# Optimization experiments

Measured on AMD Instinct MI355X. Metric: run time of the kernel, lower is better.

The kernel has to match this reference:

```python
import jax, jax.numpy as jnp
import numpy as np

N = 100000   # nodes
E = 1200000  # edges
D = 64       # input_dim
H = 64       # hidden_dim
L = 4        # num_layers (GIN layers)
G = 128      # graphs in batch
BN_EPS = 1e-5


def setup_inputs() -> dict:
    key = jax.random.key(0)
    ks = jax.random.split(key, 8)
    x = jax.random.normal(ks[0], (N, D), dtype=jnp.float32)
    edge_index = jax.random.randint(ks[1], (2, E), 0, N)
    batch = jnp.sort(jax.random.randint(ks[2], (N,), 0, G))
    s = 1.0 / np.sqrt(H).astype(np.float32)
    W_emb = jax.random.normal(ks[3], (D, H), dtype=jnp.float32) * s
    b_emb = jnp.zeros((H,), jnp.float32)
    W1 = jax.random.normal(ks[4], (L, H, H), dtype=jnp.float32) * s
    b1 = jnp.zeros((L, H), jnp.float32)
    gamma = jnp.ones((L, H), jnp.float32)
    beta = jnp.zeros((L, H), jnp.float32)
    W2 = jax.random.normal(ks[5], (L, H, H), dtype=jnp.float32) * s
    b2 = jnp.zeros((L, H), jnp.float32)
    return dict(x=x, edge_index=edge_index, batch=batch, W_emb=W_emb, b_emb=b_emb,
                W1=W1, b1=b1, gamma=gamma, beta=beta, W2=W2, b2=b2)


def _mean_pool(h, batch):
    # global_mean_pool: segment sum / segment count, fixed num_segments=G
    s = jax.ops.segment_sum(h, batch, num_segments=G)
    cnt = jax.ops.segment_sum(jnp.ones((h.shape[0],), h.dtype), batch, num_segments=G)
    return s / jnp.maximum(cnt, 1.0)[:, None]


def _bn(h, g, b):
    # BatchNorm1d in training mode: batch statistics, biased variance
    mu = h.mean(axis=0)
    var = h.var(axis=0)
    return g * (h - mu) * jax.lax.rsqrt(var + BN_EPS) + b


def reference(x, edge_index, batch, W_emb, b_emb, W1, b1, gamma, beta, W2, b2):
    src, dst = edge_index[0], edge_index[1]
    h = x @ W_emb + b_emb                      # [N, H] embedding_h
    reps = [_mean_pool(h, batch)]
    for i in range(L):
        # GINConv, eps=0: mlp((1+eps)*x + sum_{j in N(i)} x_j)
        agg = jax.ops.segment_sum(h[src], dst, num_segments=N)
        z = h + agg
        # 2-layer MLP: Linear -> BN -> ReLU -> Linear
        z = jax.nn.relu(_bn(z @ W1[i] + b1[i], gamma[i], beta[i]))
        h = z @ W2[i] + b2[i]
        reps.append(_mean_pool(h, batch))
    return jnp.concatenate(reps, axis=1)       # [G, H*(L+1)]
```

## Files before the change

### kernel.cpp

```cpp
#include <hip/hip_runtime.h>
#include <hip/hip_bf16.h>

typedef __hip_bfloat16 bf16;
typedef unsigned short u16;
typedef unsigned int u32;
typedef __attribute__((ext_vector_type(8))) short short8;
typedef __attribute__((ext_vector_type(8))) unsigned short ushort8;
typedef __attribute__((ext_vector_type(4))) float f32x4;

#define N_NODES 100000
#define N_EDGES 1200000
#define DIM 64
#define NG 128
#define NLAYERS 4
#define BN_EPS 1e-5f

#define BKT_BITS 9
#define BKT 512
#define NBKT ((N_NODES + BKT - 1) / BKT)
#define SCAT_BLK 128
#define SCAT_CH ((N_EDGES + SCAT_BLK - 1) / SCAT_BLK)
#define CSR_CAP 8192

#define WS_GSUM   0
#define WS_GSUMSQ 64
#define WS_AB     128
#define WS_FLAG   256
#define WS_GB     320
#define WS_WALL   512
#define OFF_WEMB  0
#define OFF_BEMB  4096
#define OFF_W1    4160
#define OFF_B1    20544
#define OFF_GAMMA 20800
#define OFF_BETA  21056
#define OFF_W2    21312
#define OFF_B2    37696
#define W_TOTAL   37952
#define WS_PACC8  38464
#define WS_WPK    104000
#define WS_CUR    204000
#define WS_ROWPTR 304128
#define WS_CSR    404160
#define WS_Z      1604160
#define WS_H      4804160
#define WS_PAIR   8004160
#define WS_END    9204160
#define WS_NEED_BYTES ((size_t)WS_END * 4)

#define NBLK   ((N_NODES + 63) / 64)

__device__ __forceinline__ float us2f(unsigned short u) {
    return __uint_as_float(((u32)u) << 16);
}
__device__ __forceinline__ short f2bs(float f) {
    bf16 b = __float2bfloat16(f);
    u16 u; __builtin_memcpy(&u, &b, 2);
    return (short)u;
}

__device__ __forceinline__ float loadf(const void* p, long i, int flag) {
    if (flag) return ((const float*)p)[i];
    u32 w = ((u32)((const u16*)p)[i]) << 16;
    return __uint_as_float(w);
}

__global__ void k_diag(u32* out, float val) {
    if (threadIdx.x == 0 && blockIdx.x == 0) {
        bf16 b = __float2bfloat16(val);
        u16 bits;
        __builtin_memcpy(&bits, &b, 2);
        u32 w = ((u32)bits << 16) | bits;
        for (int i = 0; i < 8; i++) out[i] = w;
    }
}

__global__ void k_detect(const void* x, int* flag) {
    if (threadIdx.x == 0 && blockIdx.x == 0) {
        const u16* u = (const u16*)x;
        int bad = 0;
        for (int i = 0; i < 512; i++) {
            float v = __uint_as_float(((u32)u[i]) << 16);
            if (!(fabsf(v) < 100.f)) bad++;
        }
        *flag = (bad > 16) ? 1 : 0;
    }
}

__global__ __launch_bounds__(256) void k_convert(const void* W_emb, const void* b_emb,
                                                 const void* W1, const void* b1,
                                                 const void* gamma, const void* beta,
                                                 const void* W2, const void* b2,
                                                 const int* flagp, float* dst) {
    int f = *flagp;
    for (int i = blockIdx.x * blockDim.x + threadIdx.x; i < W_TOTAL;
         i += gridDim.x * blockDim.x) {
        const void* p; int off;
        if (i < OFF_BEMB)       { p = W_emb; off = i; }
        else if (i < OFF_W1)    { p = b_emb; off = i - OFF_BEMB; }
        else if (i < OFF_B1)    { p = W1;    off = i - OFF_W1; }
        else if (i < OFF_GAMMA) { p = b1;    off = i - OFF_B1; }
        else if (i < OFF_BETA)  { p = gamma; off = i - OFF_GAMMA; }
        else if (i < OFF_W2)    { p = beta;  off = i - OFF_BETA; }
        else if (i < OFF_B2)    { p = W2;    off = i - OFF_W2; }
        else                    { p = b2;    off = i - OFF_B2; }
        dst[i] = loadf(p, off, f);
    }
}

__global__ __launch_bounds__(256) void k_pack(const float* __restrict__ wall,
                                              u16* __restrict__ wpk) {
    int i = blockIdx.x * 256 + threadIdx.x;
    if (i >= 9 * 4096) return;
    int m = i >> 12, r = i & 4095;
    int j = r & 7, l = (r >> 3) & 63, cc = (r >> 9) & 3, kk = r >> 11;
    int d = kk * 32 + ((l >> 4) << 3) + j;
    int c = cc * 16 + (l & 15);
    int moff = (m == 0) ? OFF_WEMB
             : (m <= 4 ? OFF_W1 + (m - 1) * 4096 : OFF_W2 + (m - 5) * 4096);
    wpk[i] = (u16)f2bs(wall[moff + d * 64 + c]);
}

__global__ void k_gbounds(const int* __restrict__ batch, int* __restrict__ gb) {
    int t = threadIdx.x;
    if (t <= NG) {
        int a = 0, b = N_NODES;
        while (a < b) { int m = (a + b) >> 1; if (batch[m] < t) a = m + 1; else b = m; }
        gb[t] = a;
    }
}


__global__ __launch_bounds__(256) void k_bhist(const int* __restrict__ ei,
                                               int* __restrict__ bhist) {
    __shared__ int hl[NBKT];
    int tid = threadIdx.x;
    for (int b = tid; b < NBKT; b += 256) hl[b] = 0;
    __syncthreads();
    for (int e = blockIdx.x * 256 + tid; e < N_EDGES; e += gridDim.x * 256)
        atomicAdd(&hl[ei[N_EDGES + e] >> BKT_BITS], 1);
    __syncthreads();
    for (int b = tid; b < NBKT; b += 256)
        if (hl[b]) atomicAdd(&bhist[b], hl[b]);
}

__global__ __launch_bounds__(256) void k_bscan(const int* __restrict__ bhist,
                                               int* __restrict__ boff,
                                               int* __restrict__ bcur) {
    __shared__ int s[256];
    int tid = threadIdx.x;
    int v = (tid < NBKT) ? bhist[tid] : 0;
    s[tid] = v;
    __syncthreads();
    for (int off = 1; off < 256; off <<= 1) {
        int t = (tid >= off) ? s[tid - off] : 0;
        __syncthreads();
        s[tid] += t;
        __syncthreads();
    }
    if (tid < NBKT) { int e = s[tid] - v; boff[tid] = e; bcur[tid] = e; }
    if (tid == 0) boff[NBKT] = s[255];
}

__global__ __launch_bounds__(256) void k_bscatter(const int* __restrict__ ei,
                                                  int* __restrict__ bcur,
                                                  u32* __restrict__ pair) {
    __shared__ int cnt[NBKT];
    int tid = threadIdx.x;
    int cbeg = blockIdx.x * SCAT_CH;
    int cend = cbeg + SCAT_CH; if (cend > N_EDGES) cend = N_EDGES;
    for (int b = tid; b < NBKT; b += 256) cnt[b] = 0;
    __syncthreads();
    for (int e = cbeg + tid; e < cend; e += 256)
        atomicAdd(&cnt[ei[N_EDGES + e] >> BKT_BITS], 1);
    __syncthreads();
    for (int b = tid; b < NBKT; b += 256) {
        int c = cnt[b];
        cnt[b] = c ? atomicAdd(&bcur[b], c) : 0;
    }
    __syncthreads();
    for (int e = cbeg + tid; e < cend; e += 256) {
        int s = ei[e];
        int d = ei[N_EDGES + e];
        int pos = atomicAdd(&cnt[d >> BKT_BITS], 1);
        pair[pos] = (u32)s | ((u32)(d & (BKT - 1)) << 17);
    }
}

__global__ __launch_bounds__(256) void k_bcsr(const u32* __restrict__ pair,
                                              const int* __restrict__ boff,
                                              int* __restrict__ rowptr,
                                              int* __restrict__ csr) {
    __shared__ int degl[BKT];
    __shared__ int offl[BKT];
    __shared__ int sc[256];
    __shared__ int csrl[CSR_CAP];
    int b = blockIdx.x, tid = threadIdx.x;
    int nbase = b << BKT_BITS;
    int nodes = N_NODES - nbase; if (nodes > BKT) nodes = BKT;
    int p0 = boff[b], p1 = boff[b + 1];
    int span = p1 - p0;
    for (int i = tid; i < BKT; i += 256) degl[i] = 0;
    __syncthreads();
    for (int p = p0 + tid; p < p1; p += 256)
        atomicAdd(&degl[pair[p] >> 17], 1);
    __syncthreads();
    int a0 = degl[2 * tid], a1 = degl[2 * tid + 1];
    sc[tid] = a0 + a1;
    __syncthreads();
    for (int off = 1; off < 256; off <<= 1) {
        int t = (tid >= off) ? sc[tid - off] : 0;
        __syncthreads();
        sc[tid] += t;
        __syncthreads();
    }
    int base = sc[tid] - (a0 + a1);
    offl[2 * tid] = base;
    offl[2 * tid + 1] = base + a0;
    __syncthreads();
    for (int i = tid; i < nodes; i += 256) rowptr[nbase + i] = p0 + offl[i];
    if (b == NBKT - 1 && tid == 0) rowptr[N_NODES] = p1;
    for (int i = tid; i < BKT; i += 256) degl[i] = offl[i];
    __syncthreads();
    if (span <= CSR_CAP) {
        for (int p = p0 + tid; p < p1; p += 256) {
            u32 pk = pair[p];
            int pos = atomicAdd(&degl[pk >> 17], 1);
            csrl[pos] = (int)(pk & 0x1FFFFu);
        }
        __syncthreads();
        for (int i = tid; i < span; i += 256) csr[p0 + i] = csrl[i];
    } else {
        for (int p = p0 + tid; p < p1; p += 256) {
            u32 pk = pair[p];
            int pos = atomicAdd(&degl[pk >> 17], 1);
            csr[p0 + pos] = (int)(pk & 0x1FFFFu);
        }
    }
}


__global__ __launch_bounds__(256) void k_deghist(const int* __restrict__ rowptr,
                                                 int* __restrict__ dhist) {
    __shared__ int hl[256];
    int tid = threadIdx.x;
    hl[tid] = 0;
    __syncthreads();
    for (int i = blockIdx.x * 256 + tid; i < N_NODES; i += gridDim.x * 256) {
        int d = rowptr[i + 1] - rowptr[i];
        int b = 255 - (d > 255 ? 255 : d);
        atomicAdd(&hl[b], 1);
    }
    __syncthreads();
    if (hl[tid]) atomicAdd(&dhist[tid], hl[tid]);
}

__global__ void k_degscan(const int* __restrict__ dhist, int* __restrict__ dhcur,
                          int* __restrict__ perm) {
    __shared__ int s[256];
    int tid = threadIdx.x;
    int v = dhist[tid];
    s[tid] = v;
    __syncthreads();
    for (int off = 1; off < 256; off <<= 1) {
        int t = (tid >= off) ? s[tid - off] : 0;
        __syncthreads();
        s[tid] += t;
        __syncthreads();
    }
    dhcur[tid] = s[tid] - v;
    if (tid < NBLK * 64 - N_NODES) perm[N_NODES + tid] = N_NODES;
}

__global__ __launch_bounds__(256) void k_degfill(const int* __restrict__ rowptr,
                                                 int* __restrict__ dhcur,
                                                 int* __restrict__ perm) {
    __shared__ int cnt[256];
    int tid = threadIdx.x;
    int chunk = (N_NODES + gridDim.x - 1) / gridDim.x;
    int beg = blockIdx.x * chunk;
    int end = beg + chunk; if (end > N_NODES) end = N_NODES;
    cnt[tid] = 0;
    __syncthreads();
    for (int i = beg + tid; i < end; i += 256) {
        int d = rowptr[i + 1] - rowptr[i];
        int b = 255 - (d > 255 ? 255 : d);
        atomicAdd(&cnt[b], 1);
    }
    __syncthreads();
    int c = cnt[tid];
    cnt[tid] = c ? atomicAdd(&dhcur[tid], c) : 0;
    __syncthreads();
    for (int i = beg + tid; i < end; i += 256) {
        int d = rowptr[i + 1] - rowptr[i];
        int b = 255 - (d > 255 ? 255 : d);
        int pos = atomicAdd(&cnt[b], 1);
        perm[pos] = i;
    }
}

__device__ __forceinline__ void store_tile(u16* cb, const f32x4* acc, bf16* out,
                                           int base, int wv, int lane) {
    int r15 = lane & 15, half = lane >> 4;
#pragma unroll
    for (int cc = 0; cc < 4; cc++) {
#pragma unroll
        for (int r = 0; r < 4; r++) {
            int trow = half * 4 + r;
            int idx = (trow * 64 + cc * 16 + r15) ^ ((trow & 7) << 3);
            cb[idx] = (u16)f2bs(acc[cc][r]);
        }
    }
#pragma unroll
    for (int p = 0; p < 2; p++) {
        int trow = lane >> 2;
        int o = (trow * 64 + (lane & 3) * 8 + p * 32) ^ ((trow & 7) << 3);
        short8 val = *(const short8*)&cb[o];
        int grow = base + (wv << 4) + trow;
        if (grow < N_NODES)
            *(short8*)((u16*)out + (long)grow * 64 + (lane & 3) * 8 + p * 32) = val;
    }
}

__device__ __forceinline__ void store_tile_p(u16* cb, const f32x4* acc, bf16* out,
                                             const int* pl, int wv, int lane) {
    int r15 = lane & 15, half = lane >> 4;
#pragma unroll
    for (int cc = 0; cc < 4; cc++) {
#pragma unroll
        for (int r = 0; r < 4; r++) {
            int trow = half * 4 + r;
            int idx = (trow * 64 + cc * 16 + r15) ^ ((trow & 7) << 3);
            cb[idx] = (u16)f2bs(acc[cc][r]);
        }
    }
#pragma unroll
    for (int p = 0; p < 2; p++) {
        int trow = lane >> 2;
        int o = (trow * 64 + (lane & 3) * 8 + p * 32) ^ ((trow & 7) << 3);
        short8 val = *(const short8*)&cb[o];
        int grow = pl[(wv << 4) + trow];
        if (grow < N_NODES)
            *(short8*)((u16*)out + (long)grow * 64 + (lane & 3) * 8 + p * 32) = val;
    }
}

__global__ __launch_bounds__(256) void k_embed(const void* __restrict__ x,
                                               const int* __restrict__ flagp,
                                               const u16* __restrict__ wpk,
                                               const float* __restrict__ bf_,
                                               bf16* __restrict__ h) {
    __shared__ u16 cbuf[4 * 1024];
    int tid = threadIdx.x, lane = tid & 63, wv = tid >> 6;
    int r15 = lane & 15, half = lane >> 4;
    int f = *flagp;
    int base = blockIdx.x * 64;
    int row = base + (wv << 4) + r15;
    bool valid = row < N_NODES;

    float xv[16];
#pragma unroll
    for (int j = 0; j < 16; j++) xv[j] = 0.f;
    if (valid) {
        if (f) {
            const f32x4* xp = (const f32x4*)((const float*)x + (long)row * 64 + half * 8);
            f32x4 u0 = xp[0], u1 = xp[1], w0 = xp[8], w1 = xp[9];
#pragma unroll
            for (int j = 0; j < 4; j++) {
                xv[j] = u0[j]; xv[4 + j] = u1[j];
                xv[8 + j] = w0[j]; xv[12 + j] = w1[j];
            }
        } else {
            const ushort8* xp = (const ushort8*)((const u16*)x + (long)row * 64 + half * 8);
            ushort8 s0 = xp[0], s1 = xp[4];
#pragma unroll
            for (int j = 0; j < 8; j++) { xv[j] = us2f(s0[j]); xv[8 + j] = us2f(s1[j]); }
        }
    }
    short8 A0, A1;
#pragma unroll
    for (int j = 0; j < 8; j++) { A0[j] = f2bs(xv[j]); A1[j] = f2bs(xv[8 + j]); }

    const short8* Wp = (const short8*)wpk;
    short8 Bw[8];
#pragma unroll
    for (int i = 0; i < 8; i++) Bw[i] = Wp[i * 64 + lane];
    f32x4 acc[4];
#pragma unroll
    for (int cc = 0; cc < 4; cc++) {
        float bb = bf_[cc * 16 + r15];
        acc[cc] = (f32x4){bb, bb, bb, bb};
        acc[cc] = __builtin_amdgcn_mfma_f32_16x16x32_bf16(A0, Bw[cc], acc[cc], 0, 0, 0);
        acc[cc] = __builtin_amdgcn_mfma_f32_16x16x32_bf16(A1, Bw[4 + cc], acc[cc], 0, 0, 0);
    }
    store_tile(cbuf + wv * 1024, acc, h, base, wv, lane);
}

__global__ __launch_bounds__(256) void k_layer1(const bf16* __restrict__ h,
                                                const int* __restrict__ rowptr,
                                                const int* __restrict__ csr,
                                                const int* __restrict__ perm,
                                                bf16* __restrict__ z,
                                                const u16* __restrict__ wpk,
                                                const float* __restrict__ bf_,
                                                float* __restrict__ gsum,
                                                float* __restrict__ gsumsq) {
    __shared__ u16 cbuf[4 * 1024];
    __shared__ float psum[DIM], psq[DIM];
    __shared__ int pl[64];
    int tid = threadIdx.x, lane = tid & 63, wv = tid >> 6;
    int r15 = lane & 15, half = lane >> 4;
    int base = blockIdx.x * 64;

    if (tid < DIM) { psum[tid] = 0.f; psq[tid] = 0.f; }
    if (tid < 64) pl[tid] = perm[base + tid];
    __syncthreads();

    int row = pl[(wv << 4) + r15];
    bool valid = row < N_NODES;

    float v[16];
#pragma unroll
    for (int j = 0; j < 16; j++) v[j] = 0.f;
    int p0 = 0, dg = 0;
    if (valid) {
        p0 = rowptr[row];
        dg = rowptr[row + 1] - p0;
        const ushort8* hp = (const ushort8*)((const u16*)h + (long)row * 64 + half * 8);
        ushort8 s0 = hp[0], s1 = hp[4];
#pragma unroll
        for (int j = 0; j < 8; j++) { v[j] = us2f(s0[j]); v[8 + j] = us2f(s1[j]); }
    }
    const int* cp = csr + p0;
    int t = 0;
    int n0 = 0, n1 = 0, n2 = 0, n3 = 0;
    if (4 <= dg) { n0 = cp[0]; n1 = cp[1]; n2 = cp[2]; n3 = cp[3]; }
    while (t + 4 <= dg) {
        const ushort8* q0 = (const ushort8*)((const u16*)h + (long)n0 * 64 + half * 8);
        const ushort8* q1 = (const ushort8*)((const u16*)h + (long)n1 * 64 + half * 8);
        const ushort8* q2 = (const ushort8*)((const u16*)h + (long)n2 * 64 + half * 8);
        const ushort8* q3 = (const ushort8*)((const u16*)h + (long)n3 * 64 + half * 8);
        ushort8 a0 = q0[0], b0 = q0[4];
        ushort8 a1 = q1[0], b1 = q1[4];
        ushort8 a2 = q2[0], b2 = q2[4];
        ushort8 a3 = q3[0], b3 = q3[4];
        t += 4;
        if (t + 4 <= dg) { n0 = cp[t]; n1 = cp[t + 1]; n2 = cp[t + 2]; n3 = cp[t + 3]; }
#pragma unroll
        for (int j = 0; j < 8; j++) {
            v[j]     += (us2f(a0[j]) + us2f(a1[j])) + (us2f(a2[j]) + us2f(a3[j]));
            v[8 + j] += (us2f(b0[j]) + us2f(b1[j])) + (us2f(b2[j]) + us2f(b3[j]));
        }
    }
    for (; t < dg; t++) {
        int s = cp[t];
        const ushort8* q = (const ushort8*)((const u16*)h + (long)s * 64 + half * 8);
        ushort8 a = q[0], b = q[4];
#pragma unroll
        for (int j = 0; j < 8; j++) { v[j] += us2f(a[j]); v[8 + j] += us2f(b[j]); }
    }

    short8 A0, A1;
#pragma unroll
    for (int j = 0; j < 8; j++) { A0[j] = f2bs(v[j]); A1[j] = f2bs(v[8 + j]); }

    const short8* Wp = (const short8*)wpk;
    short8 Bw[8];
#pragma unroll
    for (int i = 0; i < 8; i++) Bw[i] = Wp[i * 64 + lane];
    f32x4 acc[4];
#pragma unroll
    for (int cc = 0; cc < 4; cc++) {
        float bb = bf_[cc * 16 + r15];
        acc[cc] = (f32x4){bb, bb, bb, bb};
        acc[cc] = __builtin_amdgcn_mfma_f32_16x16x32_bf16(A0, Bw[cc], acc[cc], 0, 0, 0);
        acc[cc] = __builtin_amdgcn_mfma_f32_16x16x32_bf16(A1, Bw[4 + cc], acc[cc], 0, 0, 0);
    }

#pragma unroll
    for (int cc = 0; cc < 4; cc++) {
        float s = 0.f, q = 0.f;
#pragma unroll
        for (int r = 0; r < 4; r++) {
            int prow = pl[(wv << 4) + half * 4 + r];
            if (prow < N_NODES) { float val = acc[cc][r]; s += val; q += val * val; }
        }
        s += __shfl_xor(s, 16, 64); s += __shfl_xor(s, 32, 64);
        q += __shfl_xor(q, 16, 64); q += __shfl_xor(q, 32, 64);
        if (half == 0) {
            atomicAdd(&psum[cc * 16 + r15], s);
            atomicAdd(&psq[cc * 16 + r15], q);
        }
    }

    store_tile_p(cbuf + wv * 1024, acc, z, pl, wv, lane);

    __syncthreads();
    if (tid < DIM) {
        atomicAdd(&gsum[tid], psum[tid]);
        atomicAdd(&gsumsq[tid], psq[tid]);
    }
}

__global__ void k_stats(const float* __restrict__ gsum, const float* __restrict__ gsumsq,
                        const float* __restrict__ gamma_f, const float* __restrict__ beta_f,
                        float* __restrict__ ab) {
    int c = threadIdx.x;
    if (c < DIM) {
        float inv_n = 1.0f / (float)N_NODES;
        float mu = gsum[c] * inv_n;
        float var = fmaxf(gsumsq[c] * inv_n - mu * mu, 0.f);
        float a = gamma_f[c] * rsqrtf(var + BN_EPS);
        ab[c] = a;
        ab[DIM + c] = beta_f[c] - mu * a;
    }
}

__global__ __launch_bounds__(256) void k_gemm2(const bf16* __restrict__ z,
                                               bf16* __restrict__ h,
                                               const u16* __restrict__ wpk,
                                               const float* __restrict__ bf_,
                                               const float* __restrict__ ab) {
    __shared__ u16 cbuf[4 * 1024];
    int tid = threadIdx.x, lane = tid & 63, wv = tid >> 6;
    int r15 = lane & 15, half = lane >> 4;
    int base = blockIdx.x * 64;
    int row = base + (wv << 4) + r15;
    bool valid = row < N_NODES;

    const f32x4* ap = (const f32x4*)ab;
    f32x4 A0v = ap[half * 2], A1v = ap[half * 2 + 1];
    f32x4 A2v = ap[8 + half * 2], A3v = ap[8 + half * 2 + 1];
    f32x4 S0v = ap[16 + half * 2], S1v = ap[16 + half * 2 + 1];
    f32x4 S2v = ap[24 + half * 2], S3v = ap[24 + half * 2 + 1];

    float xv[16];
#pragma unroll
    for (int j = 0; j < 16; j++) xv[j] = 0.f;
    if (valid) {
        const ushort8* zp = (const ushort8*)((const u16*)z + (long)row * 64 + half * 8);
        ushort8 s0 = zp[0], s1 = zp[4];
#pragma unroll
        for (int j = 0; j < 4; j++) {
            xv[j]      = fmaxf(A0v[j] * us2f(s0[j])     + S0v[j], 0.f);
            xv[4 + j]  = fmaxf(A1v[j] * us2f(s0[4 + j]) + S1v[j], 0.f);
            xv[8 + j]  = fmaxf(A2v[j] * us2f(s1[j])     + S2v[j], 0.f);
            xv[12 + j] = fmaxf(A3v[j] * us2f(s1[4 + j]) + S3v[j], 0.f);
        }
    }
    short8 A0, A1;
#pragma unroll
    for (int j = 0; j < 8; j++) { A0[j] = f2bs(xv[j]); A1[j] = f2bs(xv[8 + j]); }

    const short8* Wp = (const short8*)wpk;
    short8 Bw[8];
#pragma unroll
    for (int i = 0; i < 8; i++) Bw[i] = Wp[i * 64 + lane];
    f32x4 acc[4];
#pragma unroll
    for (int cc = 0; cc < 4; cc++) {
        float bb = bf_[cc * 16 + r15];
        acc[cc] = (f32x4){bb, bb, bb, bb};
        acc[cc] = __builtin_amdgcn_mfma_f32_16x16x32_bf16(A0, Bw[cc], acc[cc], 0, 0, 0);
        acc[cc] = __builtin_amdgcn_mfma_f32_16x16x32_bf16(A1, Bw[4 + cc], acc[cc], 0, 0, 0);
    }
    store_tile(cbuf + wv * 1024, acc, h, base, wv, lane);
}

__global__ __launch_bounds__(256) void k_pool2(const bf16* __restrict__ h,
                                               const int* __restrict__ gb,
                                               float* __restrict__ pacc8) {
    __shared__ float ps[4][DIM];
    int g = blockIdx.x >> 3, sl = blockIdx.x & 7;
    int tid = threadIdx.x, lane = tid & 63, wv = tid >> 6;
    int chunk = lane & 7, rg = lane >> 3;
    int lo = gb[g], hi = gb[g + 1];
    float acc[8];
#pragma unroll
    for (int j = 0; j < 8; j++) acc[j] = 0.f;
    for (int r = lo + (sl * 4 + wv) * 8 + rg; r < hi; r += 256) {
        ushort8 d = *(const ushort8*)((const u16*)h + (long)r * 64 + chunk * 8);
#pragma unroll
        for (int j = 0; j < 8; j++) acc[j] += us2f(d[j]);
    }
#pragma unroll
    for (int j = 0; j < 8; j++) {
        acc[j] += __shfl_xor(acc[j], 8, 64);
        acc[j] += __shfl_xor(acc[j], 16, 64);
        acc[j] += __shfl_xor(acc[j], 32, 64);
    }
    if (rg == 0) {
#pragma unroll
        for (int j = 0; j < 8; j++) ps[wv][chunk * 8 + j] = acc[j];
    }
    __syncthreads();
    if (tid < DIM)
        pacc8[((long)g * 8 + sl) * DIM + tid] =
            ps[0][tid] + ps[1][tid] + ps[2][tid] + ps[3][tid];
}

__global__ void k_poolw(const float* __restrict__ pacc8, const int* __restrict__ gb,
                        void* __restrict__ out, int rep, const int* __restrict__ flagp) {
    int g = blockIdx.x, c = threadIdx.x;
    int f = *flagp;
    float tot = 0.f;
#pragma unroll
    for (int sl = 0; sl < 8; sl++) tot += pacc8[((long)g * 8 + sl) * DIM + c];
    tot /= fmaxf((float)(gb[g + 1] - gb[g]), 1.f);
    long idx = (long)g * (DIM * (NLAYERS + 1)) + rep * DIM + c;
    if (f) ((float*)out)[idx] = tot;
    else   ((bf16*)out)[idx] = __float2bfloat16(tot);
}

extern "C" void kernel_launch(void* const* d_in, const int* in_sizes, int n_in,
                              void* d_out, int out_size, void* d_ws, size_t ws_size,
                              hipStream_t stream) {
    static const int EXPECT[11] = {6400000, 2400000, 100000, 4096, 64,
                                   16384, 256, 256, 256, 16384, 256};
    int bad = (n_in == 11) ? -1 : 99;
    if (bad < 0)
        for (int i = 0; i < 11; i++)
            if (in_sizes[i] != EXPECT[i]) { bad = i; break; }
    if (bad >= 0) {
        k_diag<<<1, 64, 0, stream>>>((u32*)d_out, 3000.0f + 100.0f * (float)bad);
        return;
    }
    if (ws_size < WS_NEED_BYTES) {
        k_diag<<<1, 64, 0, stream>>>((u32*)d_out, 1000.0f + (float)(ws_size >> 20));
        return;
    }

    const void* x     = d_in[0];
    const int*  ei    = (const int*)d_in[1];
    const int*  batch = (const int*)d_in[2];

    float* ws = (float*)d_ws;
    float* gsum   = ws + WS_GSUM;
    float* gsumsq = ws + WS_GSUMSQ;
    float* ab     = ws + WS_AB;
    int*   flagp  = (int*)(ws + WS_FLAG);
    int*   gb     = (int*)(ws + WS_GB);
    float* WALL   = ws + WS_WALL;
    float* pacc8  = ws + WS_PACC8;
    u16*   wpk    = (u16*)(ws + WS_WPK);
    int*   curr   = (int*)(ws + WS_CUR);
    int*   bhist  = curr;
    int*   boff   = curr + 256;
    int*   bcur   = curr + 512;
    int*   dhist  = curr + 768;
    int*   dhcur  = curr + 1024;
    int*   rowptr = (int*)(ws + WS_ROWPTR);
    int*   csr    = (int*)(ws + WS_CSR);
    u32*   pair   = (u32*)(ws + WS_PAIR);
    int*   perm   = (int*)(ws + WS_PAIR);
    bf16*  z      = (bf16*)(ws + WS_Z);
    bf16*  h      = (bf16*)(ws + WS_H);

    k_detect<<<1, 64, 0, stream>>>(x, flagp);
    k_convert<<<64, 256, 0, stream>>>(d_in[3], d_in[4], d_in[5], d_in[6],
                                      d_in[7], d_in[8], d_in[9], d_in[10], flagp, WALL);
    k_pack<<<144, 256, 0, stream>>>(WALL, wpk);
    k_gbounds<<<1, 256, 0, stream>>>(batch, gb);

    hipMemsetAsync(curr, 0, 1280 * sizeof(int), stream);
    k_bhist<<<256, 256, 0, stream>>>(ei, bhist);
    k_bscan<<<1, 256, 0, stream>>>(bhist, boff, bcur);
    k_bscatter<<<SCAT_BLK, 256, 0, stream>>>(ei, bcur, pair);
    k_bcsr<<<NBKT, 256, 0, stream>>>(pair, boff, rowptr, csr);

    k_deghist<<<128, 256, 0, stream>>>(rowptr, dhist);
    k_degscan<<<1, 256, 0, stream>>>(dhist, dhcur, perm);
    k_degfill<<<128, 256, 0, stream>>>(rowptr, dhcur, perm);

    k_embed<<<NBLK, 256, 0, stream>>>(x, flagp, wpk, WALL + OFF_BEMB, h);
    k_pool2<<<NG * 8, 256, 0, stream>>>(h, gb, pacc8);
    k_poolw<<<NG, 64, 0, stream>>>(pacc8, gb, d_out, 0, flagp);
    for (int l = 0; l < NLAYERS; l++) {
        hipMemsetAsync(gsum, 0, 128 * sizeof(float), stream);
        k_layer1<<<NBLK, 256, 0, stream>>>(h, rowptr, csr, perm, z,
                                           wpk + (1 + l) * 4096,
                                           WALL + OFF_B1 + l * DIM, gsum, gsumsq);
        k_stats<<<1, 64, 0, stream>>>(gsum, gsumsq, WALL + OFF_GAMMA + l * DIM,
                                      WALL + OFF_BETA + l * DIM, ab);
        k_gemm2<<<NBLK, 256, 0, stream>>>(z, h, wpk + (5 + l) * 4096,
                                          WALL + OFF_B2 + l * DIM, ab);
        k_pool2<<<NG * 8, 256, 0, stream>>>(h, gb, pacc8);
        k_poolw<<<NG, 64, 0, stream>>>(pacc8, gb, d_out, l + 1, flagp);
    }
}
```

Baseline: 496.1 us.

## Fuse mean-pool accumulation into embed and gemm2 epilogues via atomics

Removes the separate k_pool2 pass, which re-read h after each layer, and instead accumulates per-graph sums straight from the fp32 MFMA accumulators in the k_embed and k_gemm2 epilogues. Blocks whose 64 rows all belong to one graph reduce in shared memory first; mixed blocks fall back to per-element global atomics. k_poolw now resets the pool buffer and the BN stat accumulators, which replaces the per-layer memsets. Pooling now sums fp32 values rather than bf16-rounded h, and float atomic ordering makes the sums nondeterministic.

```diff
diff --git a/kernel.cpp b/kernel.cpp
--- a/kernel.cpp
+++ b/kernel.cpp
@@ -345,18 +345,52 @@
     }
 }
 
+__device__ __forceinline__ void pool_fuse(const f32x4* acc, const int* gl, float* ps,
+                                          float* pacc, int wv, int lane, int tid) {
+    int r15 = lane & 15, half = lane >> 4;
+    if (gl[0] >= 0 && gl[0] == gl[63]) {
+#pragma unroll
+        for (int cc = 0; cc < 4; cc++) {
+            float s = (acc[cc][0] + acc[cc][1]) + (acc[cc][2] + acc[cc][3]);
+            s += __shfl_xor(s, 16, 64);
+            s += __shfl_xor(s, 32, 64);
+            if (half == 0) atomicAdd(&ps[cc * 16 + r15], s);
+        }
+        __syncthreads();
+        if (tid < DIM) atomicAdd(&pacc[(long)gl[0] * DIM + tid], ps[tid]);
+    } else {
+#pragma unroll
+        for (int r = 0; r < 4; r++) {
+            int g = gl[(wv << 4) + half * 4 + r];
+            if (g >= 0) {
+#pragma unroll
+                for (int cc = 0; cc < 4; cc++)
+                    atomicAdd(&pacc[(long)g * DIM + cc * 16 + r15], acc[cc][r]);
+            }
+        }
+    }
+}
+
 __global__ __launch_bounds__(256) void k_embed(const void* __restrict__ x,
                                                const int* __restrict__ flagp,
                                                const u16* __restrict__ wpk,
                                                const float* __restrict__ bf_,
-                                               bf16* __restrict__ h) {
+                                               bf16* __restrict__ h,
+                                               const int* __restrict__ batch,
+                                               float* __restrict__ pacc) {
     __shared__ u16 cbuf[4 * 1024];
+    __shared__ int gl[64];
+    __shared__ float ps[DIM];
     int tid = threadIdx.x, lane = tid & 63, wv = tid >> 6;
     int r15 = lane & 15, half = lane >> 4;
     int f = *flagp;
     int base = blockIdx.x * 64;
     int row = base + (wv << 4) + r15;
     bool valid = row < N_NODES;
+
+    if (tid < 64) { int rr = base + tid; gl[tid] = (rr < N_NODES) ? batch[rr] : -1; }
+    if (tid < DIM) ps[tid] = 0.f;
+    __syncthreads();
 
     float xv[16];
 #pragma unroll
@@ -394,6 +428,7 @@
         acc[cc] = __builtin_amdgcn_mfma_f32_16x16x32_bf16(A1, Bw[4 + cc], acc[cc], 0, 0, 0);
     }
     store_tile(cbuf + wv * 1024, acc, h, base, wv, lane);
+    pool_fuse(acc, gl, ps, pacc, wv, lane, tid);
 }
 
 __global__ __launch_bounds__(256) void k_layer1(const bf16* __restrict__ h,
@@ -520,14 +555,22 @@
                                                bf16* __restrict__ h,
                                                const u16* __restrict__ wpk,
                                                const float* __restrict__ bf_,
-                                               const float* __restrict__ ab) {
+                                               const float* __restrict__ ab,
+                                               const int* __restrict__ batch,
+                                               float* __restrict__ pacc) {
     __shared__ u16 cbuf[4 * 1024];
+    __shared__ int gl[64];
+    __shared__ float ps[DIM];
     int tid = threadIdx.x, lane = tid & 63, wv = tid >> 6;
     int r15 = lane & 15, half = lane >> 4;
     int base = blockIdx.x * 64;
     int row = base + (wv << 4) + r15;
     bool valid = row < N_NODES;
 
+    if (tid < 64) { int rr = base + tid; gl[tid] = (rr < N_NODES) ? batch[rr] : -1; }
+    if (tid < DIM) ps[tid] = 0.f;
+    __syncthreads();
+
     const f32x4* ap = (const f32x4*)ab;
     f32x4 A0v = ap[half * 2], A1v = ap[half * 2 + 1];
     f32x4 A2v = ap[8 + half * 2], A3v = ap[8 + half * 2 + 1];
@@ -565,51 +608,21 @@
         acc[cc] = __builtin_amdgcn_mfma_f32_16x16x32_bf16(A1, Bw[4 + cc], acc[cc], 0, 0, 0);
     }
     store_tile(cbuf + wv * 1024, acc, h, base, wv, lane);
-}
-
-__global__ __launch_bounds__(256) void k_pool2(const bf16* __restrict__ h,
-                                               const int* __restrict__ gb,
-                                               float* __restrict__ pacc8) {
-    __shared__ float ps[4][DIM];
-    int g = blockIdx.x >> 3, sl = blockIdx.x & 7;
-    int tid = threadIdx.x, lane = tid & 63, wv = tid >> 6;
-    int chunk = lane & 7, rg = lane >> 3;
-    int lo = gb[g], hi = gb[g + 1];
-    float acc[8];
-#pragma unroll
-    for (int j = 0; j < 8; j++) acc[j] = 0.f;
-    for (int r = lo + (sl * 4 + wv) * 8 + rg; r < hi; r += 256) {
-        ushort8 d = *(const ushort8*)((const u16*)h + (long)r * 64 + chunk * 8);
-#pragma unroll
-        for (int j = 0; j < 8; j++) acc[j] += us2f(d[j]);
-    }
-#pragma unroll
-    for (int j = 0; j < 8; j++) {
-        acc[j] += __shfl_xor(acc[j], 8, 64);
-        acc[j] += __shfl_xor(acc[j], 16, 64);
-        acc[j] += __shfl_xor(acc[j], 32, 64);
-    }
-    if (rg == 0) {
-#pragma unroll
-        for (int j = 0; j < 8; j++) ps[wv][chunk * 8 + j] = acc[j];
-    }
-    __syncthreads();
-    if (tid < DIM)
-        pacc8[((long)g * 8 + sl) * DIM + tid] =
-            ps[0][tid] + ps[1][tid] + ps[2][tid] + ps[3][tid];
-}
-
-__global__ void k_poolw(const float* __restrict__ pacc8, const int* __restrict__ gb,
-                        void* __restrict__ out, int rep, const int* __restrict__ flagp) {
+    pool_fuse(acc, gl, ps, pacc, wv, lane, tid);
+}
+
+__global__ void k_poolw(float* __restrict__ pacc, const int* __restrict__ gb,
+                        void* __restrict__ out, int rep, const int* __restrict__ flagp,
+                        float* __restrict__ gsum, float* __restrict__ gsumsq) {
     int g = blockIdx.x, c = threadIdx.x;
     int f = *flagp;
-    float tot = 0.f;
-#pragma unroll
-    for (int sl = 0; sl < 8; sl++) tot += pacc8[((long)g * 8 + sl) * DIM + c];
+    float tot = pacc[(long)g * DIM + c];
+    pacc[(long)g * DIM + c] = 0.f;
     tot /= fmaxf((float)(gb[g + 1] - gb[g]), 1.f);
     long idx = (long)g * (DIM * (NLAYERS + 1)) + rep * DIM + c;
     if (f) ((float*)out)[idx] = tot;
     else   ((bf16*)out)[idx] = __float2bfloat16(tot);
+    if (g == 0) { gsum[c] = 0.f; gsumsq[c] = 0.f; }
 }
 
 extern "C" void kernel_launch(void* const* d_in, const int* in_sizes, int n_in,
@@ -641,7 +654,7 @@
     int*   flagp  = (int*)(ws + WS_FLAG);
     int*   gb     = (int*)(ws + WS_GB);
     float* WALL   = ws + WS_WALL;
-    float* pacc8  = ws + WS_PACC8;
+    float* pacc   = ws + WS_PACC8;
     u16*   wpk    = (u16*)(ws + WS_WPK);
     int*   curr   = (int*)(ws + WS_CUR);
     int*   bhist  = curr;
@@ -656,6 +669,7 @@
     bf16*  z      = (bf16*)(ws + WS_Z);
     bf16*  h      = (bf16*)(ws + WS_H);
 
+    hipMemsetAsync(ws, 0, (size_t)(WS_PACC8 + NG * DIM) * 4, stream);
     k_detect<<<1, 64, 0, stream>>>(x, flagp);
     k_convert<<<64, 256, 0, stream>>>(d_in[3], d_in[4], d_in[5], d_in[6],
                                       d_in[7], d_in[8], d_in[9], d_in[10], flagp, WALL);
@@ -672,19 +686,16 @@
     k_degscan<<<1, 256, 0, stream>>>(dhist, dhcur, perm);
     k_degfill<<<128, 256, 0, stream>>>(rowptr, dhcur, perm);
 
-    k_embed<<<NBLK, 256, 0, stream>>>(x, flagp, wpk, WALL + OFF_BEMB, h);
-    k_pool2<<<NG * 8, 256, 0, stream>>>(h, gb, pacc8);
-    k_poolw<<<NG, 64, 0, stream>>>(pacc8, gb, d_out, 0, flagp);
+    k_embed<<<NBLK, 256, 0, stream>>>(x, flagp, wpk, WALL + OFF_BEMB, h, batch, pacc);
+    k_poolw<<<NG, 64, 0, stream>>>(pacc, gb, d_out, 0, flagp, gsum, gsumsq);
     for (int l = 0; l < NLAYERS; l++) {
-        hipMemsetAsync(gsum, 0, 128 * sizeof(float), stream);
         k_layer1<<<NBLK, 256, 0, stream>>>(h, rowptr, csr, perm, z,
                                            wpk + (1 + l) * 4096,
                                            WALL + OFF_B1 + l * DIM, gsum, gsumsq);
         k_stats<<<1, 64, 0, stream>>>(gsum, gsumsq, WALL + OFF_GAMMA + l * DIM,
                                       WALL + OFF_BETA + l * DIM, ab);
         k_gemm2<<<NBLK, 256, 0, stream>>>(z, h, wpk + (5 + l) * 4096,
-                                          WALL + OFF_B2 + l * DIM, ab);
-        k_pool2<<<NG * 8, 256, 0, stream>>>(h, gb, pacc8);
-        k_poolw<<<NG, 64, 0, stream>>>(pacc8, gb, d_out, l + 1, flagp);
-    }
-}
+                                          WALL + OFF_B2 + l * DIM, ab, batch, pacc);
+        k_poolw<<<NG, 64, 0, stream>>>(pacc, gb, d_out, l + 1, flagp, gsum, gsumsq);
+    }
+}
```

Result: slower. 541.2 us (+9.1%).
